# Optimization experiments

Hardware: AMD Instinct MI355X
Metric: run time of the kernel (lower is better)

Reference implementation:

```python
import jax, jax.numpy as jnp
import numpy as np

B, S, D = 4, 2048, 1024
H = 16
HD = D // H

def setup_inputs() -> dict:
    key = jax.random.key(0)
    ks = jax.random.split(key, 6)
    std = 1.0 / np.sqrt(D)
    x = jax.random.normal(ks[0], (B, S, D), dtype=jnp.float32)
    Wq = jax.random.uniform(ks[1], (D, D), jnp.float32, -std, std)
    Wk = jax.random.uniform(ks[2], (D, D), jnp.float32, -std, std)
    Wv = jax.random.uniform(ks[3], (D, D), jnp.float32, -std, std)
    Wo = jax.random.uniform(ks[4], (D, D), jnp.float32, -std, std)
    bo = jax.random.uniform(ks[5], (D,), jnp.float32, -std, std)
    return {"x": x, "Wq": Wq, "Wk": Wk, "Wv": Wv, "Wo": Wo, "bo": bo}

def reference(x, Wq, Wk, Wv, Wo, bo):
    b, s, _ = x.shape
    # projections; torch Linear computes x @ W^T, here W stored as (d_in, d_out)... we use (D, D) applied as x @ W
    q = (x @ Wq).reshape(b, s, H, HD).transpose(0, 2, 1, 3)  # b h s hd
    k = (x @ Wk).reshape(b, s, H, HD).transpose(0, 2, 1, 3)
    v = (x @ Wv).reshape(b, s, H, HD).transpose(0, 2, 1, 3)
    scores = jnp.einsum('bhqd,bhkd->bhqk', q, k)
    causal = jnp.triu(jnp.ones((s, s), dtype=bool), k=1)
    scores = jnp.where(causal[None, None], -jnp.inf, scores)
    attn = jax.nn.softmax(scores / np.sqrt(HD), axis=-1)  # dropout=0.0 -> identity
    ctx = jnp.einsum('bhqk,bhkd->bhqd', attn, v)
    ctx = ctx.transpose(0, 2, 1, 3).reshape(b, s, D)
    return ctx @ Wo + bo
```

## Files before the change

### kernel.cpp

```cpp
#include <hip/hip_runtime.h>

typedef unsigned short u16;
typedef __bf16 bf16x8 __attribute__((ext_vector_type(8)));
typedef float f32x4 __attribute__((ext_vector_type(4)));

#define Bn 4
#define Sn 2048
#define Dn 1024
#define Hn 16
#define HDn 64

__device__ inline u16 f2bf(float f) {
  unsigned u = __builtin_bit_cast(unsigned, f);
  u += 0x7fffu + ((u >> 16) & 1u);
  return (u16)(u >> 16);
}

__device__ __forceinline__ void gl2lds16(const u16* g, u16* l) {
  __builtin_amdgcn_global_load_lds(
      (const __attribute__((address_space(1))) unsigned int*)g,
      (__attribute__((address_space(3))) unsigned int*)l, 16, 0, 0);
}

__device__ __forceinline__ float fexp2(float x) {
  return __builtin_amdgcn_exp2f(x);
}

__device__ __forceinline__ unsigned pk_bf_trunc(float lo, float hi) {
  return __builtin_amdgcn_perm(__builtin_bit_cast(unsigned, hi),
                               __builtin_bit_cast(unsigned, lo), 0x07060302u);
}

__global__ __launch_bounds__(256) void cvt4(const float* __restrict__ in,
                                            u16* __restrict__ out, int n4) {
  int i = blockIdx.x * 256 + threadIdx.x;
  if (i < n4) {
    float4 v = ((const float4*)in)[i];
    ushort4 o;
    o.x = f2bf(v.x); o.y = f2bf(v.y); o.z = f2bf(v.z); o.w = f2bf(v.w);
    ((ushort4*)out)[i] = o;
  }
}

__global__ __launch_bounds__(256) void tcvt4(const float* __restrict__ w0,
                                             const float* __restrict__ w1,
                                             const float* __restrict__ w2,
                                             const float* __restrict__ w3,
                                             u16* __restrict__ out) {
  __shared__ u16 tile[32][33];
  const float* in = (blockIdx.z == 0) ? w0 : (blockIdx.z == 1) ? w1
                   : (blockIdx.z == 2) ? w2 : w3;
  u16* dst = out + (size_t)blockIdx.z * Dn * Dn;
  int bx = blockIdx.x * 32;
  int by = blockIdx.y * 32;
  int tx = threadIdx.x & 31;
  int ty = threadIdx.x >> 5;
#pragma unroll
  for (int r = 0; r < 32; r += 8)
    tile[ty + r][tx] = f2bf(in[(size_t)(by + ty + r) * Dn + bx + tx]);
  __syncthreads();
#pragma unroll
  for (int r = 0; r < 32; r += 8)
    dst[(size_t)(bx + ty + r) * Dn + by + tx] = tile[tx][ty + r];
}

__global__ __launch_bounds__(256) void gemm_qkv(const u16* __restrict__ A,
                                                const u16* __restrict__ Bt,
                                                u16* __restrict__ qkb,
                                                u16* __restrict__ vt,
                                                float qscale) {
  __shared__ __attribute__((aligned(16))) u16 As[2][2][128][32];
  __shared__ __attribute__((aligned(16))) u16 Bs[2][2][128][32];
  const int K = Dn;
  const int t = threadIdx.x;
  const int wave = t >> 6;
  const int lane = t & 63;
  const int lcol = lane & 15;
  const int quad = lane >> 4;
  const int wm = (wave >> 1) * 64;
  const int wn = (wave & 1) * 64;
  const int bm = blockIdx.y * 128;
  const int bn = blockIdx.x * 128;

  const int srow = lane >> 2;
  const int sseg = (lane & 3) * 8;
  const u16* a0p = A + (size_t)(bm + wave * 16 + srow) * K + sseg;
  const u16* a1p = a0p + (size_t)64 * K;
  const u16* b0p = Bt + (size_t)(bn + wave * 16 + srow) * K + sseg;
  const u16* b1p = b0p + (size_t)64 * K;
  u16* asl = &As[0][0][0][0] + wave * 512 + lane * 8;
  u16* bsl = &Bs[0][0][0][0] + wave * 512 + lane * 8;

  auto stage = [&](int k0, int d) {
    u16* as = asl + d * 8192;
    u16* bs = bsl + d * 8192;
    gl2lds16(a0p + k0, as);
    gl2lds16(a1p + k0, as + 2048);
    gl2lds16(a0p + k0 + 32, as + 4096);
    gl2lds16(a1p + k0 + 32, as + 6144);
    gl2lds16(b0p + k0, bs);
    gl2lds16(b1p + k0, bs + 2048);
    gl2lds16(b0p + k0 + 32, bs + 4096);
    gl2lds16(b1p + k0 + 32, bs + 6144);
  };

  f32x4 acc[4][4];
#pragma unroll
  for (int i = 0; i < 4; i++)
#pragma unroll
    for (int j = 0; j < 4; j++) acc[i][j] = (f32x4){0.f, 0.f, 0.f, 0.f};

  stage(0, 0);
  int d = 0;
  for (int k0 = 0; k0 < K; k0 += 64, d ^= 1) {
    __syncthreads();
    if (k0 + 64 < K) stage(k0 + 64, d ^ 1);
#pragma unroll
    for (int ks = 0; ks < 2; ks++) {
      bf16x8 af[4], bf[4];
#pragma unroll
      for (int mi = 0; mi < 4; mi++)
        af[mi] = *(const bf16x8*)(&As[d][ks][wm + mi * 16 + lcol][quad * 8]);
#pragma unroll
      for (int ni = 0; ni < 4; ni++)
        bf[ni] = *(const bf16x8*)(&Bs[d][ks][wn + ni * 16 + lcol][quad * 8]);
#pragma unroll
      for (int mi = 0; mi < 4; mi++)
#pragma unroll
        for (int ni = 0; ni < 4; ni++)
          acc[mi][ni] = __builtin_amdgcn_mfma_f32_16x16x32_bf16(af[mi], bf[ni], acc[mi][ni], 0, 0, 0);
    }
  }

  if (bn >= 2048) {
    const int b = bm >> 11;
#pragma unroll
    for (int mi = 0; mi < 4; mi++) {
#pragma unroll
      for (int ni = 0; ni < 4; ni++) {
        int row0 = bm + wm + mi * 16 + quad * 4;
        int s = row0 & (Sn - 1);
        int vcol = bn + wn + ni * 16 + lcol - 2048;
        int bh = (b << 4) + (vcol >> 6);
        int hd = vcol & 63;
        unsigned d0 = (unsigned)f2bf(acc[mi][ni][0]) |
                      ((unsigned)f2bf(acc[mi][ni][1]) << 16);
        unsigned d1 = (unsigned)f2bf(acc[mi][ni][2]) |
                      ((unsigned)f2bf(acc[mi][ni][3]) << 16);
        *(uint2*)(vt + ((size_t)bh * HDn + hd) * Sn + s) = (uint2){d0, d1};
      }
    }
  } else {
    const float scale = (bn < 1024) ? qscale : 1.0f;
#pragma unroll
    for (int mi = 0; mi < 4; mi++) {
#pragma unroll
      for (int ni = 0; ni < 4; ni++) {
#pragma unroll
        for (int r = 0; r < 4; r++) {
          int row = bm + wm + mi * 16 + quad * 4 + r;
          int col = bn + wn + ni * 16 + lcol;
          qkb[(size_t)row * 2048 + col] = f2bf(acc[mi][ni][r] * scale);
        }
      }
    }
  }
}

__global__ __launch_bounds__(256) void gemm_out(const u16* __restrict__ A,
                                                const u16* __restrict__ Bt,
                                                float* __restrict__ Cout,
                                                const float* __restrict__ bias) {
  __shared__ __attribute__((aligned(16))) u16 As[2][2][128][32];
  __shared__ __attribute__((aligned(16))) u16 Bs[2][2][128][32];
  const int K = Dn;
  const int t = threadIdx.x;
  const int wave = t >> 6;
  const int lane = t & 63;
  const int lcol = lane & 15;
  const int quad = lane >> 4;
  const int wm = (wave >> 1) * 64;
  const int wn = (wave & 1) * 64;
  const int bm = blockIdx.y * 128;
  const int bn = blockIdx.x * 128;

  const int srow = lane >> 2;
  const int sseg = (lane & 3) * 8;
  const u16* a0p = A + (size_t)(bm + wave * 16 + srow) * K + sseg;
  const u16* a1p = a0p + (size_t)64 * K;
  const u16* b0p = Bt + (size_t)(bn + wave * 16 + srow) * K + sseg;
  const u16* b1p = b0p + (size_t)64 * K;
  u16* asl = &As[0][0][0][0] + wave * 512 + lane * 8;
  u16* bsl = &Bs[0][0][0][0] + wave * 512 + lane * 8;

  auto stage = [&](int k0, int d) {
    u16* as = asl + d * 8192;
    u16* bs = bsl + d * 8192;
    gl2lds16(a0p + k0, as);
    gl2lds16(a1p + k0, as + 2048);
    gl2lds16(a0p + k0 + 32, as + 4096);
    gl2lds16(a1p + k0 + 32, as + 6144);
    gl2lds16(b0p + k0, bs);
    gl2lds16(b1p + k0, bs + 2048);
    gl2lds16(b0p + k0 + 32, bs + 4096);
    gl2lds16(b1p + k0 + 32, bs + 6144);
  };

  f32x4 acc[4][4];
#pragma unroll
  for (int i = 0; i < 4; i++)
#pragma unroll
    for (int j = 0; j < 4; j++) acc[i][j] = (f32x4){0.f, 0.f, 0.f, 0.f};

  stage(0, 0);
  int d = 0;
  for (int k0 = 0; k0 < K; k0 += 64, d ^= 1) {
    __syncthreads();
    if (k0 + 64 < K) stage(k0 + 64, d ^ 1);
#pragma unroll
    for (int ks = 0; ks < 2; ks++) {
      bf16x8 af[4], bf[4];
#pragma unroll
      for (int mi = 0; mi < 4; mi++)
        af[mi] = *(const bf16x8*)(&As[d][ks][wm + mi * 16 + lcol][quad * 8]);
#pragma unroll
      for (int ni = 0; ni < 4; ni++)
        bf[ni] = *(const bf16x8*)(&Bs[d][ks][wn + ni * 16 + lcol][quad * 8]);
#pragma unroll
      for (int mi = 0; mi < 4; mi++)
#pragma unroll
        for (int ni = 0; ni < 4; ni++)
          acc[mi][ni] = __builtin_amdgcn_mfma_f32_16x16x32_bf16(af[mi], bf[ni], acc[mi][ni], 0, 0, 0);
    }
  }

#pragma unroll
  for (int mi = 0; mi < 4; mi++) {
#pragma unroll
    for (int ni = 0; ni < 4; ni++) {
#pragma unroll
      for (int r = 0; r < 4; r++) {
        int row = bm + wm + mi * 16 + quad * 4 + r;
        int col = bn + wn + ni * 16 + lcol;
        Cout[(size_t)row * Dn + col] = acc[mi][ni][r] + bias[col];
      }
    }
  }
}

__global__ __launch_bounds__(256, 2) void attn5(const u16* __restrict__ QK,
                                                const u16* __restrict__ Vt,
                                                u16* __restrict__ ctx) {
  __shared__ __attribute__((aligned(16))) u16 Ks2[2][64][32];
  __shared__ __attribute__((aligned(16))) u16 Vts2[2][64][32];
  __shared__ __attribute__((aligned(16))) u16 Pt[4][32][72];

  const int bh = blockIdx.x;
  const int b = bh >> 4, h = bh & 15;
  const int pair = blockIdx.y;
  const int t = threadIdx.x;
  const int w = t >> 6;
  const int lane = t & 63;
  const int lcol = lane & 15;
  const int quad = lane >> 4;
  const int qw0 = pair * 128 + w * 32;
  const int qw1 = (15 - pair) * 128 + w * 32;

  const size_t qkbase = ((size_t)b * Sn) * 2048 + h * HDn;
  const size_t obase = ((size_t)b * Sn) * Dn + h * HDn;
  const size_t vbase = ((size_t)bh * HDn) * Sn;

  bf16x8 qf[2][2][2];
#pragma unroll
  for (int si = 0; si < 2; si++) {
    const int qws = si ? qw1 : qw0;
#pragma unroll
    for (int qb = 0; qb < 2; qb++) {
      const u16* qp = QK + qkbase + (size_t)(qws + qb * 16 + lcol) * 2048 + quad * 8;
      qf[si][qb][0] = *(const bf16x8*)qp;
      qf[si][qb][1] = *(const bf16x8*)(qp + 32);
    }
  }

  f32x4 o[2][2][4];
#pragma unroll
  for (int si = 0; si < 2; si++)
#pragma unroll
    for (int qb = 0; qb < 2; qb++)
#pragma unroll
      for (int nb = 0; nb < 4; nb++) o[si][qb][nb] = (f32x4){0.f, 0.f, 0.f, 0.f};
  float lsum[2][2] = {{0.f, 0.f}, {0.f, 0.f}};

  const int srow = lane >> 2;
  const int sseg = (lane & 3) * 8;
  const u16* kp0 = QK + qkbase + 1024 + (size_t)(w * 16 + srow) * 2048 + sseg;
  const u16* vp0 = Vt + vbase + (size_t)(w * 16 + srow) * Sn + sseg;
  u16* ksl0 = &Ks2[0][0][0] + w * 512 + lane * 8;
  u16* ksl1 = ksl0 + 2048;
  u16* vsl0 = &Vts2[0][0][0] + w * 512 + lane * 8;
  u16* vsl1 = vsl0 + 2048;

  auto do_strip = [&](int si, int qw, int j0) {
    f32x4 s[4][2];
#pragma unroll
    for (int mb = 0; mb < 4; mb++) {
      bf16x8 kf0 = *(const bf16x8*)(&Ks2[0][mb * 16 + lcol][quad * 8]);
      bf16x8 kf1 = *(const bf16x8*)(&Ks2[1][mb * 16 + lcol][quad * 8]);
#pragma unroll
      for (int qb = 0; qb < 2; qb++) {
        f32x4 a = (f32x4){0.f, 0.f, 0.f, 0.f};
        a = __builtin_amdgcn_mfma_f32_16x16x32_bf16(kf0, qf[si][qb][0], a, 0, 0, 0);
        a = __builtin_amdgcn_mfma_f32_16x16x32_bf16(kf1, qf[si][qb][1], a, 0, 0, 0);
        s[mb][qb] = a;
      }
    }

    const bool needmask = (j0 + 63 > qw);
#pragma unroll
    for (int qb = 0; qb < 2; qb++) {
      const int qrow = qw + qb * 16 + lcol;
#pragma unroll
      for (int mb = 0; mb < 4; mb++) {
        float p[4];
#pragma unroll
        for (int r = 0; r < 4; r++) p[r] = fexp2(s[mb][qb][r]);
        if (needmask) {
          const int kvb = j0 + mb * 16 + quad * 4;
#pragma unroll
          for (int r = 0; r < 4; r++)
            if (kvb + r > qrow) p[r] = 0.f;
        }
        lsum[si][qb] += (p[0] + p[1]) + (p[2] + p[3]);
        unsigned d0 = pk_bf_trunc(p[0], p[1]);
        unsigned d1 = pk_bf_trunc(p[2], p[3]);
        *(uint2*)(&Pt[w][qb * 16 + lcol][mb * 16 + quad * 4]) = (uint2){d0, d1};
      }
    }

#pragma unroll
    for (int c = 0; c < 2; c++) {
      bf16x8 pf0 = *(const bf16x8*)(&Pt[w][lcol][c * 32 + quad * 8]);
      bf16x8 pf1 = *(const bf16x8*)(&Pt[w][16 + lcol][c * 32 + quad * 8]);
#pragma unroll
      for (int nb = 0; nb < 4; nb++) {
        bf16x8 vf = *(const bf16x8*)(&Vts2[c][nb * 16 + lcol][quad * 8]);
        o[si][0][nb] = __builtin_amdgcn_mfma_f32_16x16x32_bf16(vf, pf0, o[si][0][nb], 0, 0, 0);
        o[si][1][nb] = __builtin_amdgcn_mfma_f32_16x16x32_bf16(vf, pf1, o[si][1][nb], 0, 0, 0);
      }
    }
  };

  const int n_kv = (15 - pair) * 128 + 128;

  for (int j0 = 0; j0 < n_kv; j0 += 64) {
    {
      const u16* kp = kp0 + (size_t)j0 * 2048;
      gl2lds16(kp, ksl0);
      gl2lds16(kp + 32, ksl1);
      const u16* vp = vp0 + j0;
      gl2lds16(vp, vsl0);
      gl2lds16(vp + 32, vsl1);
    }
    __syncthreads();

    if (j0 <= qw1 + 31) do_strip(1, qw1, j0);
    if (j0 <= qw0 + 31) do_strip(0, qw0, j0);
    __syncthreads();
  }

#pragma unroll
  for (int si = 0; si < 2; si++) {
    const int qws = si ? qw1 : qw0;
#pragma unroll
    for (int qb = 0; qb < 2; qb++) {
      float l = lsum[si][qb];
      l += __shfl_xor(l, 16);
      l += __shfl_xor(l, 32);
      float inv = 1.0f / l;
#pragma unroll
      for (int nb = 0; nb < 4; nb++) {
        unsigned d0 = (unsigned)f2bf(o[si][qb][nb][0] * inv) |
                      ((unsigned)f2bf(o[si][qb][nb][1] * inv) << 16);
        unsigned d1 = (unsigned)f2bf(o[si][qb][nb][2] * inv) |
                      ((unsigned)f2bf(o[si][qb][nb][3] * inv) << 16);
        u16* p = ctx + obase + (size_t)(qws + qb * 16 + lcol) * Dn + nb * 16 + quad * 4;
        *(uint2*)p = (uint2){d0, d1};
      }
    }
  }
}

extern "C" void kernel_launch(void* const* d_in, const int* in_sizes, int n_in,
                              void* d_out, int out_size, void* d_ws, size_t ws_size,
                              hipStream_t stream) {
  const float* x  = (const float*)d_in[0];
  const float* Wq = (const float*)d_in[1];
  const float* Wk = (const float*)d_in[2];
  const float* Wv = (const float*)d_in[3];
  const float* Wo = (const float*)d_in[4];
  const float* bo = (const float*)d_in[5];
  float* out = (float*)d_out;

  const size_t BSD = (size_t)Bn * Sn * Dn;
  const size_t DD = (size_t)Dn * Dn;

  u16* xb    = (u16*)d_ws;
  u16* wall  = xb + BSD;
  u16* qkb   = wall + 4 * DD;
  u16* vt    = qkb + 2 * BSD;
  u16* cb    = vt + BSD;

  cvt4<<<(int)(BSD / 4 / 256), 256, 0, stream>>>(x, xb, (int)(BSD / 4));
  tcvt4<<<dim3(Dn / 32, Dn / 32, 4), 256, 0, stream>>>(Wq, Wk, Wv, Wo, wall);

  gemm_qkv<<<dim3(3072 / 128, (Bn * Sn) / 128), 256, 0, stream>>>(
      xb, wall, qkb, vt, 0.125f * 1.44269504f);

  attn5<<<dim3(Bn * Hn, 8), 256, 0, stream>>>(qkb, vt, cb);

  gemm_out<<<dim3(Dn / 128, (Bn * Sn) / 128), 256, 0, stream>>>(cb, wall + 3 * DD, out, bo);
}
```

Baseline: 236.6 us.

## Rewrite QKV GEMM with 256x256 tiles, 8 waves, swizzled LDS and phased pipeline

The QKV projection GEMM moves from 128x128 tiles with 4 waves to 256x256 tiles with 8 waves per 512-thread block, launched as a 1D grid of 384 blocks with a block-index swizzle for L2 locality. LDS is split into four quarter-tile regions per buffer with an XOR swizzle to avoid bank conflicts. The K loop runs as eight phases per iteration that interleave global-to-LDS staging with MFMA work, using explicit vmcnt waits, barriers and setprio. The aim is more data reuse per loaded byte and better overlap of loads with math, at the cost of higher register and LDS use and only 384 blocks to spread across the CUs.

```diff
diff --git a/kernel.cpp b/kernel.cpp
--- a/kernel.cpp
+++ b/kernel.cpp
@@ -64,104 +64,150 @@
     dst[(size_t)(bx + ty + r) * Dn + by + tx] = tile[tx][ty + r];
 }
 
-__global__ __launch_bounds__(256) void gemm_qkv(const u16* __restrict__ A,
-                                                const u16* __restrict__ Bt,
-                                                u16* __restrict__ qkb,
-                                                u16* __restrict__ vt,
-                                                float qscale) {
-  __shared__ __attribute__((aligned(16))) u16 As[2][2][128][32];
-  __shared__ __attribute__((aligned(16))) u16 Bs[2][2][128][32];
-  const int K = Dn;
-  const int t = threadIdx.x;
-  const int wave = t >> 6;
-  const int lane = t & 63;
+__global__ __launch_bounds__(512, 2) void gemm_qkv(const u16* __restrict__ A,
+                                                   const u16* __restrict__ Bt,
+                                                   u16* __restrict__ qkb,
+                                                   u16* __restrict__ vt,
+                                                   float qscale) {
+  __shared__ __attribute__((aligned(16))) u16 S[2][4][8192];
+
+  const int tid = threadIdx.x;
+  const int lane = tid & 63;
   const int lcol = lane & 15;
   const int quad = lane >> 4;
-  const int wm = (wave >> 1) * 64;
-  const int wn = (wave & 1) * 64;
-  const int bm = blockIdx.y * 128;
-  const int bn = blockIdx.x * 128;
-
-  const int srow = lane >> 2;
-  const int sseg = (lane & 3) * 8;
-  const u16* a0p = A + (size_t)(bm + wave * 16 + srow) * K + sseg;
-  const u16* a1p = a0p + (size_t)64 * K;
-  const u16* b0p = Bt + (size_t)(bn + wave * 16 + srow) * K + sseg;
-  const u16* b1p = b0p + (size_t)64 * K;
-  u16* asl = &As[0][0][0][0] + wave * 512 + lane * 8;
-  u16* bsl = &Bs[0][0][0][0] + wave * 512 + lane * 8;
-
-  auto stage = [&](int k0, int d) {
-    u16* as = asl + d * 8192;
-    u16* bs = bsl + d * 8192;
-    gl2lds16(a0p + k0, as);
-    gl2lds16(a1p + k0, as + 2048);
-    gl2lds16(a0p + k0 + 32, as + 4096);
-    gl2lds16(a1p + k0 + 32, as + 6144);
-    gl2lds16(b0p + k0, bs);
-    gl2lds16(b1p + k0, bs + 2048);
-    gl2lds16(b0p + k0 + 32, bs + 4096);
-    gl2lds16(b1p + k0 + 32, bs + 6144);
+  const int wave = tid >> 6;
+  const int wr = wave >> 2;
+  const int wc = wave & 3;
+
+  const int bid = blockIdx.x;
+  const int swz = (bid & 7) * 48 + (bid >> 3);
+  const int bm = (swz & 31) * 256;
+  const int bn = (swz >> 5) * 256;
+
+  const u16* srcp[4][2];
+#pragma unroll
+  for (int rg = 0; rg < 4; rg++) {
+#pragma unroll
+    for (int j = 0; j < 2; j++) {
+      int o = j * 8192 + tid * 16;
+      int l = o ^ (((o >> 8) & 7) << 4);
+      int rho = l >> 7;
+      int c2 = (l >> 1) & 63;
+      int gr;
+      if (rg == 0)      gr = bm + (rho & 63) + ((rho >> 6) << 7);
+      else if (rg == 1) gr = bm + 64 + (rho & 63) + ((rho >> 6) << 7);
+      else if (rg == 2) gr = bn + ((rho >> 5) << 6) + (rho & 31);
+      else              gr = bn + ((rho >> 5) << 6) + 32 + (rho & 31);
+      const u16* base = (rg < 2) ? A : Bt;
+      srcp[rg][j] = base + (size_t)gr * Dn + c2;
+    }
+  }
+
+  auto stg = [&](int rg, int buf, int tile) {
+    if (tile >= 16) return;
+    const int k0 = tile << 6;
+    u16* d = &S[buf][rg][tid * 8];
+    gl2lds16(srcp[rg][0] + k0, d);
+    gl2lds16(srcp[rg][1] + k0, d + 4096);
   };
 
-  f32x4 acc[4][4];
-#pragma unroll
-  for (int i = 0; i < 4; i++)
+  f32x4 acc[8][4];
+#pragma unroll
+  for (int i = 0; i < 8; i++)
 #pragma unroll
     for (int j = 0; j < 4; j++) acc[i][j] = (f32x4){0.f, 0.f, 0.f, 0.f};
 
-  stage(0, 0);
-  int d = 0;
-  for (int k0 = 0; k0 < K; k0 += 64, d ^= 1) {
-    __syncthreads();
-    if (k0 + 64 < K) stage(k0 + 64, d ^ 1);
-#pragma unroll
-    for (int ks = 0; ks < 2; ks++) {
-      bf16x8 af[4], bf[4];
-#pragma unroll
-      for (int mi = 0; mi < 4; mi++)
-        af[mi] = *(const bf16x8*)(&As[d][ks][wm + mi * 16 + lcol][quad * 8]);
-#pragma unroll
-      for (int ni = 0; ni < 4; ni++)
-        bf[ni] = *(const bf16x8*)(&Bs[d][ks][wn + ni * 16 + lcol][quad * 8]);
-#pragma unroll
-      for (int mi = 0; mi < 4; mi++)
-#pragma unroll
-        for (int ni = 0; ni < 4; ni++)
-          acc[mi][ni] = __builtin_amdgcn_mfma_f32_16x16x32_bf16(af[mi], bf[ni], acc[mi][ni], 0, 0, 0);
-    }
-  }
-
+  const int SW = (lcol & 14) << 3;
+  const int cs0 = (quad * 16) ^ SW;
+  const int cs1 = (64 + quad * 16) ^ SW;
+
+#define PHASE(BUF, QR, QC, STG_STMT, WAIT_STMT)                               \
+  {                                                                           \
+    const char* Ab = (const char*)&S[BUF][QR][0];                             \
+    const char* Bb = (const char*)&S[BUF][2 + QC][0];                         \
+    bf16x8 af0[4], af1[4], bf0[2], bf1[2];                                    \
+    _Pragma("unroll") for (int mi = 0; mi < 4; mi++) {                        \
+      int r = (wr * 64 + mi * 16 + lcol) * 128;                               \
+      af0[mi] = *(const bf16x8*)(Ab + (r + cs0));                             \
+      af1[mi] = *(const bf16x8*)(Ab + (r + cs1));                             \
+    }                                                                         \
+    _Pragma("unroll") for (int ni = 0; ni < 2; ni++) {                        \
+      int r = (wc * 32 + ni * 16 + lcol) * 128;                               \
+      bf0[ni] = *(const bf16x8*)(Bb + (r + cs0));                             \
+      bf1[ni] = *(const bf16x8*)(Bb + (r + cs1));                             \
+    }                                                                         \
+    STG_STMT;                                                                 \
+    WAIT_STMT;                                                                \
+    __builtin_amdgcn_s_barrier();                                             \
+    asm volatile("s_waitcnt lgkmcnt(0)" ::: "memory");                        \
+    __builtin_amdgcn_sched_barrier(0);                                        \
+    __builtin_amdgcn_s_setprio(1);                                            \
+    _Pragma("unroll") for (int mi = 0; mi < 4; mi++)                          \
+      _Pragma("unroll") for (int ni = 0; ni < 2; ni++) {                      \
+        acc[QR * 4 + mi][QC * 2 + ni] =                                       \
+            __builtin_amdgcn_mfma_f32_16x16x32_bf16(                          \
+                af0[mi], bf0[ni], acc[QR * 4 + mi][QC * 2 + ni], 0, 0, 0);    \
+        acc[QR * 4 + mi][QC * 2 + ni] =                                       \
+            __builtin_amdgcn_mfma_f32_16x16x32_bf16(                          \
+                af1[mi], bf1[ni], acc[QR * 4 + mi][QC * 2 + ni], 0, 0, 0);    \
+      }                                                                       \
+    __builtin_amdgcn_s_setprio(0);                                            \
+    __builtin_amdgcn_s_barrier();                                             \
+  }
+
+  stg(0, 0, 0); stg(2, 0, 0); stg(1, 0, 0); stg(3, 0, 0);
+  stg(0, 1, 1); stg(2, 1, 1);
+  asm volatile("s_waitcnt vmcnt(4)" ::: "memory");
+  __builtin_amdgcn_s_barrier();
+
+#pragma unroll 1
+  for (int I = 0; I < 8; ++I) {
+    const int t1 = 2 * I + 1, t2 = 2 * I + 2, t3 = 2 * I + 3;
+    PHASE(0, 0, 0, stg(1, 1, t1), );
+    PHASE(0, 0, 1, stg(3, 1, t1), );
+    PHASE(0, 1, 0, stg(0, 0, t2), );
+    PHASE(0, 1, 1, stg(2, 0, t2),
+          if (I < 7) asm volatile("s_waitcnt vmcnt(4)" ::: "memory");
+          else asm volatile("s_waitcnt vmcnt(0)" ::: "memory"));
+    PHASE(1, 0, 0, stg(1, 0, t2), );
+    PHASE(1, 0, 1, stg(3, 0, t2), );
+    PHASE(1, 1, 0, stg(0, 1, t3), );
+    PHASE(1, 1, 1, stg(2, 1, t3),
+          if (I < 7) asm volatile("s_waitcnt vmcnt(4)" ::: "memory"));
+  }
+#undef PHASE
+
+  const int rb = bm + wr * 128 + quad * 4;
+  const int cb = bn + wc * 64 + lcol;
   if (bn >= 2048) {
-    const int b = bm >> 11;
-#pragma unroll
-    for (int mi = 0; mi < 4; mi++) {
-#pragma unroll
-      for (int ni = 0; ni < 4; ni++) {
-        int row0 = bm + wm + mi * 16 + quad * 4;
+#pragma unroll
+    for (int ai = 0; ai < 8; ai++) {
+#pragma unroll
+      for (int bj = 0; bj < 4; bj++) {
+        int row0 = rb + ((ai >> 2) << 6) + ((ai & 3) << 4);
         int s = row0 & (Sn - 1);
-        int vcol = bn + wn + ni * 16 + lcol - 2048;
-        int bh = (b << 4) + (vcol >> 6);
+        int bb = row0 >> 11;
+        int vcol = cb + ((bj >> 1) << 5) + ((bj & 1) << 4) - 2048;
+        int bh = (bb << 4) + (vcol >> 6);
         int hd = vcol & 63;
-        unsigned d0 = (unsigned)f2bf(acc[mi][ni][0]) |
-                      ((unsigned)f2bf(acc[mi][ni][1]) << 16);
-        unsigned d1 = (unsigned)f2bf(acc[mi][ni][2]) |
-                      ((unsigned)f2bf(acc[mi][ni][3]) << 16);
+        unsigned d0 = (unsigned)f2bf(acc[ai][bj][0]) |
+                      ((unsigned)f2bf(acc[ai][bj][1]) << 16);
+        unsigned d1 = (unsigned)f2bf(acc[ai][bj][2]) |
+                      ((unsigned)f2bf(acc[ai][bj][3]) << 16);
         *(uint2*)(vt + ((size_t)bh * HDn + hd) * Sn + s) = (uint2){d0, d1};
       }
     }
   } else {
     const float scale = (bn < 1024) ? qscale : 1.0f;
 #pragma unroll
-    for (int mi = 0; mi < 4; mi++) {
-#pragma unroll
-      for (int ni = 0; ni < 4; ni++) {
-#pragma unroll
-        for (int r = 0; r < 4; r++) {
-          int row = bm + wm + mi * 16 + quad * 4 + r;
-          int col = bn + wn + ni * 16 + lcol;
-          qkb[(size_t)row * 2048 + col] = f2bf(acc[mi][ni][r] * scale);
-        }
+    for (int ai = 0; ai < 8; ai++) {
+#pragma unroll
+      for (int bj = 0; bj < 4; bj++) {
+        int row0 = rb + ((ai >> 2) << 6) + ((ai & 3) << 4);
+        int col = cb + ((bj >> 1) << 5) + ((bj & 1) << 4);
+#pragma unroll
+        for (int r = 0; r < 4; r++)
+          qkb[(size_t)(row0 + r) * 2048 + col] = f2bf(acc[ai][bj][r] * scale);
       }
     }
   }
@@ -413,8 +459,8 @@
   cvt4<<<(int)(BSD / 4 / 256), 256, 0, stream>>>(x, xb, (int)(BSD / 4));
   tcvt4<<<dim3(Dn / 32, Dn / 32, 4), 256, 0, stream>>>(Wq, Wk, Wv, Wo, wall);
 
-  gemm_qkv<<<dim3(3072 / 128, (Bn * Sn) / 128), 256, 0, stream>>>(
-      xb, wall, qkb, vt, 0.125f * 1.44269504f);
+  gemm_qkv<<<dim3(384), 512, 0, stream>>>(xb, wall, qkb, vt,
+                                          0.125f * 1.44269504f);
 
   attn5<<<dim3(Bn * Hn, 8), 256, 0, stream>>>(qkb, vt, cb);
 
```

Result: slower. 253.3 us (+7.0%).
